# Performance work log

Hardware: AMD Instinct MI355X
Metric: run time of the kernel (lower is better)

Reference implementation:

```python
import jax, jax.numpy as jnp
import numpy as np

N, C, EB, ES = 200000, 2000, 2000000, 40000
LATENT, HIDDEN, EMB = 128, 512, 16
EPS = 1e-4

def _ln(x, g, b):
    m = jnp.mean(x, -1, keepdims=True)
    v = jnp.var(x, -1, keepdims=True)
    return (x - m) / jnp.sqrt(v + 1e-5) * g + b

def _l2norm(x):
    return x / jnp.maximum(jnp.linalg.norm(x, axis=-1, keepdims=True), 1e-12)

def setup_inputs():
    key = jax.random.key(0)
    ks = jax.random.split(key, 10)
    def w(k, shape):
        return jax.random.normal(k, shape, jnp.float32) / np.sqrt(shape[0]).astype(np.float32)
    return dict(
        nodes=jax.random.normal(ks[0], (N, LATENT), jnp.float32),
        clusters=jax.random.randint(ks[1], (N,), 0, C),
        bip_src=jax.random.randint(ks[2], (EB,), 0, N),
        bip_dst=jax.random.randint(ks[3], (EB,), 0, C),
        sup_src=jax.random.randint(ks[4], (ES,), 0, C),
        sup_dst=jax.random.randint(ks[5], (ES,), 0, C),
        cW1=w(ks[6], (LATENT, HIDDEN)), cb1=jnp.zeros((HIDDEN,), jnp.float32),
        cg1=jnp.ones((HIDDEN,), jnp.float32), cbe1=jnp.zeros((HIDDEN,), jnp.float32),
        cW2=w(ks[7], (HIDDEN, EMB)), cb2=jnp.zeros((EMB,), jnp.float32),
        eW1=w(ks[8], (2 * LATENT, HIDDEN)), eb1=jnp.zeros((HIDDEN,), jnp.float32),
        eg1=jnp.ones((HIDDEN,), jnp.float32), ebe1=jnp.zeros((HIDDEN,), jnp.float32),
        eW2=w(ks[9], (HIDDEN, LATENT)), eb2=jnp.zeros((LATENT,), jnp.float32),
        eg2=jnp.ones((LATENT,), jnp.float32), ebe2=jnp.zeros((LATENT,), jnp.float32),
    )

def _forward(nodes, cW1, cb1, cg1, cbe1, cW2, cb2,
             eW1, eb1, eg1, ebe1, eW2, eb2, eg2, ebe2,
             clusters, bip_src, bip_dst, sup_src, sup_dst):
    # clustering network (Linear-LN-ReLU-Linear) + L2 normalize -> [N, EMB]
    emb = jax.nn.relu(_ln(nodes @ cW1 + cb1, cg1, cbe1)) @ cW2 + cb2
    emb = _l2norm(emb)
    # scatter-mean of embeddings per cluster -> supernode centers [C, EMB]
    valid = clusters >= 0
    wgt = valid.astype(emb.dtype)
    cl = jnp.where(valid, clusters, 0)
    sums = jax.ops.segment_sum(emb * wgt[:, None], cl, num_segments=C)
    cnt = jax.ops.segment_sum(wgt, cl, num_segments=C)
    means = _l2norm(sums / jnp.maximum(cnt, 1.0)[:, None])
    # bipartite attention: dot products per edge, min/max-normalized softmax
    # grouped by source node (segment id = bip_src, dim_size = N)
    att = jnp.sum(emb[bip_src] * means[bip_dst], axis=-1)
    amax = jax.ops.segment_max(att, bip_src, num_segments=N)[bip_src]
    amin = jax.ops.segment_min(att, bip_src, num_segments=N)[bip_src]
    att = jnp.exp(2.0 * (att - amin) / (EPS + jax.lax.stop_gradient(amax - amin)))
    bip_att = (att / (EPS + jax.ops.segment_sum(att, bip_src, num_segments=N)[bip_src]))[:, None]
    # supergraph attention: tanh of min/max-normalized dot products,
    # grouped by destination supernode (segment id = sup_dst, dim_size = C)
    satt = jnp.sum(means[sup_src] * means[sup_dst], axis=-1)
    smax = jax.ops.segment_max(satt, sup_dst, num_segments=C)[sup_dst]
    smin = jax.ops.segment_min(satt, sup_dst, num_segments=C)[sup_dst]
    satt = jnp.tanh(2.0 * (satt - smin) / (EPS + jax.lax.stop_gradient(smax - smin)))[:, None]
    # scatter-add raw node features into supernodes, weighted by attention
    supernodes = jax.ops.segment_sum(nodes[bip_src] * bip_att, bip_dst, num_segments=C)
    # superedge encoder (Linear-LN-ReLU-Linear-LN-ReLU) on endpoint concat
    se_in = jnp.concatenate([supernodes[sup_src], supernodes[sup_dst]], axis=1)
    h = jax.nn.relu(_ln(se_in @ eW1 + eb1, eg1, ebe1))
    superedges = jax.nn.relu(_ln(h @ eW2 + eb2, eg2, ebe2))
    return supernodes, superedges, bip_att, satt

def reference(nodes, clusters, bip_src, bip_dst, sup_src, sup_dst,
              cW1, cb1, cg1, cbe1, cW2, cb2,
              eW1, eb1, eg1, ebe1, eW2, eb2, eg2, ebe2):
    return _forward(nodes, cW1, cb1, cg1, cbe1, cW2, cb2,
                    eW1, eb1, eg1, ebe1, eW2, eb2, eg2, ebe2,
                    clusters, bip_src, bip_dst, sup_src, sup_dst)
```

## Files before the change

kernel.cpp:

```cpp
#include <hip/hip_runtime.h>

#define NN 200000
#define CC 2000
#define EBN 2000000
#define ESN 40000
#define EPSA 1e-4f
#define SCH 8000
#define NBKT 1563
#define CVB 1056
#define HSB 977

typedef unsigned short ushort_t;
typedef float f32x4 __attribute__((ext_vector_type(4)));
typedef __bf16 bf16x8 __attribute__((ext_vector_type(8)));
typedef _Float16 f16x8 __attribute__((ext_vector_type(8)));

__device__ __forceinline__ unsigned fenc(float f) {
    unsigned b = __float_as_uint(f);
    return (b & 0x80000000u) ? ~b : (b | 0x80000000u);
}
__device__ __forceinline__ float fdec(unsigned u) {
    return (u & 0x80000000u) ? __uint_as_float(u ^ 0x80000000u) : __uint_as_float(~u);
}
__device__ __forceinline__ unsigned f2bf(float f) {
    unsigned u = __float_as_uint(f);
    return (u + 0x7fffu + ((u >> 16) & 1u)) >> 16;
}
__device__ __forceinline__ float bf2f(ushort_t u) { return __uint_as_float(((unsigned)u) << 16); }
__device__ __forceinline__ ushort_t f2h(float f) {
    const _Float16 h = (_Float16)f;
    return __builtin_bit_cast(ushort_t, h);
}
__device__ __forceinline__ float dot16(const ushort_t* __restrict__ emb_h, const float* __restrict__ means,
                                       int s, int d) {
    const uint4 e0v = *(const uint4*)(emb_h + (size_t)s * 16);
    const uint4 e1v = *(const uint4*)(emb_h + (size_t)s * 16 + 8);
    const float4* mv = (const float4*)(means + (size_t)d * 16);
    const float4 m0 = mv[0], m1 = mv[1], m2 = mv[2], m3 = mv[3];
    float dot = 0.f;
    dot += bf2f((ushort_t)(e0v.x & 0xFFFF)) * m0.x + bf2f((ushort_t)(e0v.x >> 16)) * m0.y;
    dot += bf2f((ushort_t)(e0v.y & 0xFFFF)) * m0.z + bf2f((ushort_t)(e0v.y >> 16)) * m0.w;
    dot += bf2f((ushort_t)(e0v.z & 0xFFFF)) * m1.x + bf2f((ushort_t)(e0v.z >> 16)) * m1.y;
    dot += bf2f((ushort_t)(e0v.w & 0xFFFF)) * m1.z + bf2f((ushort_t)(e0v.w >> 16)) * m1.w;
    dot += bf2f((ushort_t)(e1v.x & 0xFFFF)) * m2.x + bf2f((ushort_t)(e1v.x >> 16)) * m2.y;
    dot += bf2f((ushort_t)(e1v.y & 0xFFFF)) * m2.z + bf2f((ushort_t)(e1v.y >> 16)) * m2.w;
    dot += bf2f((ushort_t)(e1v.z & 0xFFFF)) * m3.x + bf2f((ushort_t)(e1v.z >> 16)) * m3.y;
    dot += bf2f((ushort_t)(e1v.w & 0xFFFF)) * m3.z + bf2f((ushort_t)(e1v.w >> 16)) * m3.w;
    return dot;
}

__global__ __launch_bounds__(256) void k_setup(const float* __restrict__ cW1, const float* __restrict__ cW2,
                                               const float* __restrict__ eW1, const float* __restrict__ eW2,
                                               ushort_t* __restrict__ cW1h, ushort_t* __restrict__ cW2h,
                                               ushort_t* __restrict__ eW1t, ushort_t* __restrict__ eW2t,
                                               const int* __restrict__ bsrc, const int* __restrict__ bdst,
                                               int* __restrict__ hist_d, int* __restrict__ hist_s) {
    __shared__ int hd[CC];
    __shared__ int hs[NBKT];
    if (blockIdx.x < CVB) {
        int id = blockIdx.x * 256 + threadIdx.x;
        if (id < 65536) {
            const int n = id >> 7, k = id & 127;
            cW1h[id] = f2h(cW1[k * 512 + n]);
            return;
        }
        id -= 65536;
        if (id < 8192) {
            const int n = id >> 9, k = id & 511;
            cW2h[id] = f2h(cW2[k * 16 + n]);
            return;
        }
        id -= 8192;
        if (id < 131072) { const int n = id >> 8, k = id & 255; eW1t[id] = (ushort_t)f2bf(eW1[k * 512 + n]); return; }
        id -= 131072;
        if (id < 65536) { const int n = id >> 9, k = id & 511; eW2t[id] = (ushort_t)f2bf(eW2[k * 128 + n]); return; }
        return;
    }
    const int t = threadIdx.x;
    for (int i = t; i < CC; i += 256) hd[i] = 0;
    for (int i = t; i < NBKT; i += 256) hs[i] = 0;
    __syncthreads();
    for (int e = (blockIdx.x - CVB) * 256 + t; e < EBN; e += HSB * 256) {
        atomicAdd(&hd[bdst[e]], 1);
        atomicAdd(&hs[bsrc[e] >> 7], 1);
    }
    __syncthreads();
    for (int i = t; i < CC; i += 256) if (hd[i]) atomicAdd(&hist_d[i], hd[i]);
    for (int i = t; i < NBKT; i += 256) if (hs[i]) atomicAdd(&hist_s[i], hs[i]);
}

__global__ __launch_bounds__(1024) void k_scan2(const int* __restrict__ hist_d, int* __restrict__ offs_d,
                                                int* __restrict__ cursor_d, const int* __restrict__ hist_s,
                                                int* __restrict__ offs_s, int* __restrict__ cursor_s) {
    const int* hist = blockIdx.x ? hist_s : hist_d;
    int* offs = blockIdx.x ? offs_s : offs_d;
    int* cursor = blockIdx.x ? cursor_s : cursor_d;
    const int n = blockIdx.x ? NBKT : CC;
    __shared__ int buf[2][2048];
    const int t = threadIdx.x;
    buf[0][t]        = (t        < n) ? hist[t]        : 0;
    buf[0][t + 1024] = (t + 1024 < n) ? hist[t + 1024] : 0;
    __syncthreads();
    int pp = 0;
    for (int off = 1; off < 2048; off <<= 1) {
        const int np = pp ^ 1;
        for (int i = t; i < 2048; i += 1024) {
            int v = buf[pp][i];
            if (i >= off) v += buf[pp][i - off];
            buf[np][i] = v;
        }
        pp = np;
        __syncthreads();
    }
    for (int i = t; i < n; i += 1024) {
        const int ex = (i == 0) ? 0 : buf[pp][i - 1];
        offs[i] = ex;
        cursor[i] = ex;
    }
}

__global__ __launch_bounds__(256, 3) void k_mlp1(
    const float* __restrict__ nodes, const int* __restrict__ clusters,
    const ushort_t* __restrict__ W1h, const float* __restrict__ b1,
    const float* __restrict__ g1, const float* __restrict__ be1,
    const ushort_t* __restrict__ W2h, const float* __restrict__ b2,
    ushort_t* __restrict__ emb_h, float* __restrict__ sums, float* __restrict__ cnt,
    ushort_t* __restrict__ nodes_h) {
    __shared__ char Ubuf[16384];
    __shared__ float redS[4][32], redQ[4][32];
    ushort_t* Xh = (ushort_t*)Ubuf;
    const int tid = threadIdx.x;
    const int row0 = blockIdx.x * 32;

#pragma unroll
    for (int i = 0; i < 2; ++i) {
        const int c = tid + 256 * i;
        const int row = c >> 4, c8 = c & 15;
        const float4* gp = (const float4*)(nodes + (size_t)(row0 + row) * 128 + c8 * 8);
        const float4 u = gp[0], v = gp[1];
        uint4 pkh;
        pkh.x = f2h(u.x) | ((unsigned)f2h(u.y) << 16);
        pkh.y = f2h(u.z) | ((unsigned)f2h(u.w) << 16);
        pkh.z = f2h(v.x) | ((unsigned)f2h(v.y) << 16);
        pkh.w = f2h(v.z) | ((unsigned)f2h(v.w) << 16);
        const int byte = row * 256 + ((c8 * 16) ^ ((row & 7) << 4));
        *(uint4*)((char*)Xh + byte) = pkh;
        if (nodes_h) {
            uint4 pkb;
            pkb.x = f2bf(u.x) | (f2bf(u.y) << 16);
            pkb.y = f2bf(u.z) | (f2bf(u.w) << 16);
            pkb.z = f2bf(v.x) | (f2bf(v.y) << 16);
            pkb.w = f2bf(v.z) | (f2bf(v.w) << 16);
            ((uint4*)nodes_h)[(size_t)(row0 + row) * 16 + c8] = pkb;
        }
    }
    __syncthreads();

    const int wv = tid >> 6, l = tid & 63;
    const int q = l >> 4, c16 = l & 15;
    const int wcol0 = wv * 128;

    f32x4 acc[2][8];
#pragma unroll
    for (int mt = 0; mt < 2; ++mt)
#pragma unroll
        for (int nt = 0; nt < 8; ++nt) acc[mt][nt] = (f32x4){0.f, 0.f, 0.f, 0.f};

#pragma unroll
    for (int ks = 0; ks < 4; ++ks) {
        f16x8 ah[2];
#pragma unroll
        for (int mt = 0; mt < 2; ++mt) {
            const int row = 16 * mt + c16;
            const int byte = row * 256 + ((64 * ks + 16 * q) ^ ((row & 7) << 4));
            ah[mt] = __builtin_bit_cast(f16x8, *(const uint4*)((const char*)Xh + byte));
        }
#pragma unroll
        for (int nt = 0; nt < 8; ++nt) {
            const int n = wcol0 + 16 * nt + c16;
            const f16x8 bh = __builtin_bit_cast(f16x8, *(const uint4*)(W1h + n * 128 + 32 * ks + 8 * q));
#pragma unroll
            for (int mt = 0; mt < 2; ++mt)
                acc[mt][nt] = __builtin_amdgcn_mfma_f32_16x16x32_f16(ah[mt], bh, acc[mt][nt], 0, 0, 0);
        }
    }

    float b1v[8], g1v[8], bev[8];
#pragma unroll
    for (int nt = 0; nt < 8; ++nt) {
        const int col = wcol0 + 16 * nt + c16;
        b1v[nt] = b1[col]; g1v[nt] = g1[col]; bev[nt] = be1[col];
    }
    float sS[2][4], sQ[2][4];
#pragma unroll
    for (int mt = 0; mt < 2; ++mt)
#pragma unroll
        for (int r = 0; r < 4; ++r) {
            float s = 0.f, qq = 0.f;
#pragma unroll
            for (int nt = 0; nt < 8; ++nt) {
                const float h = acc[mt][nt][r] + b1v[nt];
                acc[mt][nt][r] = h;
                s += h; qq += h * h;
            }
#pragma unroll
            for (int off = 1; off < 16; off <<= 1) {
                s += __shfl_xor(s, off);
                qq += __shfl_xor(qq, off);
            }
            sS[mt][r] = s; sQ[mt][r] = qq;
        }
    if (c16 == 0) {
#pragma unroll
        for (int mt = 0; mt < 2; ++mt)
#pragma unroll
            for (int r = 0; r < 4; ++r) {
                const int row = 16 * mt + 4 * q + r;
                redS[wv][row] = sS[mt][r];
                redQ[wv][row] = sQ[mt][r];
            }
    }
    __syncthreads();

    float mean[2][4], inv[2][4];
#pragma unroll
    for (int mt = 0; mt < 2; ++mt)
#pragma unroll
        for (int r = 0; r < 4; ++r) {
            const int row = 16 * mt + 4 * q + r;
            const float S = redS[0][row] + redS[1][row] + redS[2][row] + redS[3][row];
            const float Q = redQ[0][row] + redQ[1][row] + redQ[2][row] + redQ[3][row];
            const float m_ = S * (1.f / 512.f);
            mean[mt][r] = m_;
            inv[mt][r] = rsqrtf(Q * (1.f / 512.f) - m_ * m_ + 1e-5f);
        }

    ushort_t* Hw = (ushort_t*)(Ubuf + 8192 + wv * 2048);
    f32x4 acc2[2];
    acc2[0] = (f32x4){0.f, 0.f, 0.f, 0.f};
    acc2[1] = (f32x4){0.f, 0.f, 0.f, 0.f};
#pragma unroll
    for (int ch = 0; ch < 4; ++ch) {
#pragma unroll
        for (int mt = 0; mt < 2; ++mt)
#pragma unroll
            for (int r = 0; r < 4; ++r) {
                const int row = 16 * mt + 4 * q + r;
                const int swz = (((row >> 2) & 1) << 3) | (((row >> 3) & 1) << 4);
#pragma unroll
                for (int ntl = 0; ntl < 2; ++ntl) {
                    const int nt = 2 * ch + ntl;
                    const float rv = fmaxf((acc[mt][nt][r] - mean[mt][r]) * inv[mt][r] * g1v[nt] + bev[nt], 0.f);
                    Hw[row * 32 + ((16 * ntl + c16) ^ swz)] = f2h(rv);
                }
            }
        const int kg = wcol0 + 32 * ch + 8 * q;
        const f16x8 bh = __builtin_bit_cast(f16x8, *(const uint4*)(W2h + c16 * 512 + kg));
#pragma unroll
        for (int mt = 0; mt < 2; ++mt) {
            const int row = 16 * mt + c16;
            const int swz = (((row >> 2) & 1) << 3) | (((row >> 3) & 1) << 4);
            const int ci = (8 * q) ^ swz;
            const f16x8 ah = __builtin_bit_cast(f16x8, *(const uint4*)(Hw + row * 32 + ci));
            acc2[mt] = __builtin_amdgcn_mfma_f32_16x16x32_f16(ah, bh, acc2[mt], 0, 0, 0);
        }
    }
    __syncthreads();

    float* Cb = (float*)Ubuf;
#pragma unroll
    for (int mt = 0; mt < 2; ++mt)
#pragma unroll
        for (int r = 0; r < 4; ++r) Cb[(wv * 32 + 16 * mt + 4 * q + r) * 16 + c16] = acc2[mt][r];
    __syncthreads();

#pragma unroll
    for (int rep = 0; rep < 2; ++rep) {
        const int slot = tid + 256 * rep;
        const int row = slot >> 4, col = slot & 15;
        float val = Cb[(0 * 32 + row) * 16 + col] + Cb[(1 * 32 + row) * 16 + col] +
                    Cb[(2 * 32 + row) * 16 + col] + Cb[(3 * 32 + row) * 16 + col] + b2[col];
        float ss = val * val;
#pragma unroll
        for (int off = 1; off < 16; off <<= 1) ss += __shfl_xor(ss, off);
        const float ev = val / fmaxf(sqrtf(ss), 1e-12f);
        const int grow = row0 + row;
        emb_h[(size_t)grow * 16 + col] = (ushort_t)f2bf(ev);
        const int cl = clusters[grow];
        if (cl >= 0) {
            atomicAdd(&sums[cl * 16 + col], ev);
            if (col == 0) atomicAdd(&cnt[cl], 1.f);
        }
    }
}

__global__ __launch_bounds__(256) void k_means(const float* __restrict__ sums, const float* __restrict__ cnt,
                                               float* __restrict__ means) {
    const int t = blockIdx.x * 256 + threadIdx.x;
    const int c = t >> 4;
    const float v = sums[t] / fmaxf(cnt[c], 1.f);
    float sq = v * v;
#pragma unroll
    for (int off = 1; off < 16; off <<= 1) sq += __shfl_xor(sq, off, 16);
    means[t] = v / fmaxf(sqrtf(sq), 1e-12f);
}

__global__ __launch_bounds__(512) void k_bip_sort(const int* __restrict__ src, int* __restrict__ cursor_s,
                                                  unsigned* __restrict__ eid_s) {
    __shared__ int h[NBKT];
    __shared__ int base[NBKT];
    const int t = threadIdx.x;
    const int e0 = blockIdx.x * SCH;
    for (int i = t; i < NBKT; i += 512) h[i] = 0;
    __syncthreads();
    for (int i = t; i < SCH; i += 512) atomicAdd(&h[src[e0 + i] >> 7], 1);
    __syncthreads();
    for (int i = t; i < NBKT; i += 512) {
        const int c = h[i];
        if (c) base[i] = atomicAdd(&cursor_s[i], c);
        h[i] = 0;
    }
    __syncthreads();
    for (int i = t; i < SCH; i += 512) {
        const int e = e0 + i;
        const int s = src[e];
        const int b = s >> 7;
        const int rank = atomicAdd(&h[b], 1);
        eid_s[base[b] + rank] = ((unsigned)(s & 127) << 21) | (unsigned)e;
    }
}

__global__ __launch_bounds__(512) void k_bip_seg(const unsigned* __restrict__ eid_s, const int* __restrict__ offs_s,
                                                 const int* __restrict__ hist_s,
                                                 const int* __restrict__ bdst, const ushort_t* __restrict__ emb_h,
                                                 const float* __restrict__ means, float* __restrict__ att) {
    const int b = blockIdx.x, t = threadIdx.x;
    const int base = offs_s[b], n = hist_s[b];
    const int s0 = b << 7;
    __shared__ unsigned mxs[128], mns[128];
    __shared__ float sms[128];
    if (t < 128) { mxs[t] = 0u; mns[t] = 0xFFFFFFFFu; sms[t] = 0.f; }
    __syncthreads();
    float dv[8];
    int sl[8], ev[8];
#pragma unroll
    for (int k = 0; k < 8; ++k) {
        const int i = k * 512 + t;
        if (i < n) {
            const unsigned pk = eid_s[base + i];
            const int e = (int)(pk & 0x1FFFFFu);
            const int slv = (int)(pk >> 21);
            const int d = bdst[e];
            const float dot = dot16(emb_h, means, s0 + slv, d);
            dv[k] = dot; sl[k] = slv; ev[k] = e;
            const unsigned enc = fenc(dot);
            atomicMax(&mxs[slv], enc);
            atomicMin(&mns[slv], enc);
        }
    }
    for (int i = 4096 + t; i < n; i += 512) {
        const unsigned pk = eid_s[base + i];
        const int e = (int)(pk & 0x1FFFFFu);
        const int slv = (int)(pk >> 21);
        const float dot = dot16(emb_h, means, s0 + slv, bdst[e]);
        const unsigned enc = fenc(dot);
        atomicMax(&mxs[slv], enc);
        atomicMin(&mns[slv], enc);
    }
    __syncthreads();
#pragma unroll
    for (int k = 0; k < 8; ++k) {
        const int i = k * 512 + t;
        if (i < n) {
            const float mx = fdec(mxs[sl[k]]), mn = fdec(mns[sl[k]]);
            const float a = __expf(2.f * (dv[k] - mn) / (EPSA + (mx - mn)));
            dv[k] = a;
            atomicAdd(&sms[sl[k]], a);
        }
    }
    for (int i = 4096 + t; i < n; i += 512) {
        const unsigned pk = eid_s[base + i];
        const int e = (int)(pk & 0x1FFFFFu);
        const int slv = (int)(pk >> 21);
        const float dot = dot16(emb_h, means, s0 + slv, bdst[e]);
        const float mx = fdec(mxs[slv]), mn = fdec(mns[slv]);
        atomicAdd(&sms[slv], __expf(2.f * (dot - mn) / (EPSA + (mx - mn))));
    }
    __syncthreads();
#pragma unroll
    for (int k = 0; k < 8; ++k) {
        const int i = k * 512 + t;
        if (i < n) att[ev[k]] = dv[k] / (EPSA + sms[sl[k]]);
    }
    for (int i = 4096 + t; i < n; i += 512) {
        const unsigned pk = eid_s[base + i];
        const int e = (int)(pk & 0x1FFFFFu);
        const int slv = (int)(pk >> 21);
        const float dot = dot16(emb_h, means, s0 + slv, bdst[e]);
        const float mx = fdec(mxs[slv]), mn = fdec(mns[slv]);
        const float a = __expf(2.f * (dot - mn) / (EPSA + (mx - mn)));
        att[e] = a / (EPSA + sms[slv]);
    }
}

__global__ __launch_bounds__(512) void k_bip_scatter(const int* __restrict__ src, const int* __restrict__ dst,
                                                     const float* __restrict__ att,
                                                     int* __restrict__ cursor, int* __restrict__ src_sorted,
                                                     ushort_t* __restrict__ w_sorted) {
    __shared__ int h[CC];
    __shared__ int base[CC];
    const int t = threadIdx.x;
    const int e0 = blockIdx.x * SCH;
    for (int i = t; i < CC; i += 512) h[i] = 0;
    __syncthreads();
    for (int i = t; i < SCH; i += 512) atomicAdd(&h[dst[e0 + i]], 1);
    __syncthreads();
    for (int i = t; i < CC; i += 512) {
        const int c = h[i];
        if (c) base[i] = atomicAdd(&cursor[i], c);
        h[i] = 0;
    }
    __syncthreads();
    for (int i = t; i < SCH; i += 512) {
        const int e = e0 + i;
        const int s = src[e], d = dst[e];
        const float w = att[e];
        const int rank = atomicAdd(&h[d], 1);
        const int pos = base[d] + rank;
        src_sorted[pos] = s;
        w_sorted[pos] = (ushort_t)f2bf(w);
    }
}

__global__ __launch_bounds__(256) void k_supernode_h(const int* __restrict__ src_sorted,
                                                     const ushort_t* __restrict__ w_sorted,
                                                     const int* __restrict__ offs, const int* __restrict__ hist,
                                                     const ushort_t* __restrict__ nodes_h,
                                                     float* __restrict__ out_sn) {
    const int c = blockIdx.x, t = threadIdx.x;
    const int base = offs[c], n = hist[c];
    const int slot = t >> 5, lane = t & 31;
    const ushort4* nh4 = (const ushort4*)nodes_h;
    float4 aA = make_float4(0.f, 0.f, 0.f, 0.f);
    float4 aB = make_float4(0.f, 0.f, 0.f, 0.f);
    float4 aC = make_float4(0.f, 0.f, 0.f, 0.f);
    float4 aD = make_float4(0.f, 0.f, 0.f, 0.f);
    int i0 = 0;
    for (; i0 + 32 <= n; i0 += 32) {
        {
            const int idx = base + i0 + slot;
            const float w = bf2f(w_sorted[idx]);
            const ushort4 v = nh4[(size_t)src_sorted[idx] * 32 + lane];
            aA.x = fmaf(w, bf2f(v.x), aA.x); aA.y = fmaf(w, bf2f(v.y), aA.y);
            aA.z = fmaf(w, bf2f(v.z), aA.z); aA.w = fmaf(w, bf2f(v.w), aA.w);
        }
        {
            const int idx = base + i0 + 8 + slot;
            const float w = bf2f(w_sorted[idx]);
            const ushort4 v = nh4[(size_t)src_sorted[idx] * 32 + lane];
            aB.x = fmaf(w, bf2f(v.x), aB.x); aB.y = fmaf(w, bf2f(v.y), aB.y);
            aB.z = fmaf(w, bf2f(v.z), aB.z); aB.w = fmaf(w, bf2f(v.w), aB.w);
        }
        {
            const int idx = base + i0 + 16 + slot;
            const float w = bf2f(w_sorted[idx]);
            const ushort4 v = nh4[(size_t)src_sorted[idx] * 32 + lane];
            aC.x = fmaf(w, bf2f(v.x), aC.x); aC.y = fmaf(w, bf2f(v.y), aC.y);
            aC.z = fmaf(w, bf2f(v.z), aC.z); aC.w = fmaf(w, bf2f(v.w), aC.w);
        }
        {
            const int idx = base + i0 + 24 + slot;
            const float w = bf2f(w_sorted[idx]);
            const ushort4 v = nh4[(size_t)src_sorted[idx] * 32 + lane];
            aD.x = fmaf(w, bf2f(v.x), aD.x); aD.y = fmaf(w, bf2f(v.y), aD.y);
            aD.z = fmaf(w, bf2f(v.z), aD.z); aD.w = fmaf(w, bf2f(v.w), aD.w);
        }
    }
    for (; i0 < n; i0 += 8) {
        if (i0 + slot < n) {
            const int idx = base + i0 + slot;
            const float w = bf2f(w_sorted[idx]);
            const ushort4 v = nh4[(size_t)src_sorted[idx] * 32 + lane];
            aA.x = fmaf(w, bf2f(v.x), aA.x); aA.y = fmaf(w, bf2f(v.y), aA.y);
            aA.z = fmaf(w, bf2f(v.z), aA.z); aA.w = fmaf(w, bf2f(v.w), aA.w);
        }
    }
    __shared__ float4 red[256];
    red[t] = make_float4((aA.x + aB.x) + (aC.x + aD.x), (aA.y + aB.y) + (aC.y + aD.y),
                         (aA.z + aB.z) + (aC.z + aD.z), (aA.w + aB.w) + (aC.w + aD.w));
    __syncthreads();
    if (t < 32) {
        float4 r = red[t];
#pragma unroll
        for (int k2 = 1; k2 < 8; ++k2) {
            const float4 o = red[t + 32 * k2];
            r.x += o.x; r.y += o.y; r.z += o.z; r.w += o.w;
        }
        ((float4*)(out_sn + (size_t)c * 128))[t] = r;
    }
}

__global__ __launch_bounds__(256) void k_supernode(const int* __restrict__ src_sorted,
                                                   const ushort_t* __restrict__ w_sorted,
                                                   const int* __restrict__ offs, const int* __restrict__ hist,
                                                   const float* __restrict__ nodes, float* __restrict__ out_sn) {
    const int c = blockIdx.x, t = threadIdx.x;
    const int base = offs[c], n = hist[c];
    const int slot = t >> 5, lane = t & 31;
    const float4* nodes4 = (const float4*)nodes;
    float4 aA = make_float4(0.f, 0.f, 0.f, 0.f);
    int i0 = 0;
    for (; i0 < n; i0 += 8) {
        if (i0 + slot < n) {
            const int idx = base + i0 + slot;
            const float w = bf2f(w_sorted[idx]);
            const float4 v = nodes4[(size_t)src_sorted[idx] * 32 + lane];
            aA.x = fmaf(w, v.x, aA.x); aA.y = fmaf(w, v.y, aA.y);
            aA.z = fmaf(w, v.z, aA.z); aA.w = fmaf(w, v.w, aA.w);
        }
    }
    __shared__ float4 red[256];
    red[t] = aA;
    __syncthreads();
    if (t < 32) {
        float4 r = red[t];
#pragma unroll
        for (int k2 = 1; k2 < 8; ++k2) {
            const float4 o = red[t + 32 * k2];
            r.x += o.x; r.y += o.y; r.z += o.z; r.w += o.w;
        }
        ((float4*)(out_sn + (size_t)c * 128))[t] = r;
    }
}

__global__ __launch_bounds__(256) void k_sup_dot(const int* __restrict__ ss, const int* __restrict__ sd,
                                                 const float* __restrict__ means, float* __restrict__ satt,
                                                 unsigned* __restrict__ smax, unsigned* __restrict__ smin) {
    const int e = blockIdx.x * 256 + threadIdx.x;
    if (e >= ESN) return;
    const int s = ss[e], d = sd[e];
    const float4* av = (const float4*)(means + (size_t)s * 16);
    const float4* bv = (const float4*)(means + (size_t)d * 16);
    float dot = 0.f;
#pragma unroll
    for (int q = 0; q < 4; ++q) {
        const float4 a = av[q], b = bv[q];
        dot += a.x * b.x + a.y * b.y + a.z * b.z + a.w * b.w;
    }
    satt[e] = dot;
    const unsigned enc = fenc(dot);
    atomicMax(&smax[d], enc);
    atomicMin(&smin[d], enc);
}

__global__ __launch_bounds__(256) void k_sup_tanh(const int* __restrict__ sd, float* __restrict__ satt,
                                                  const unsigned* __restrict__ smax,
                                                  const unsigned* __restrict__ smin) {
    const int e = blockIdx.x * 256 + threadIdx.x;
    if (e >= ESN) return;
    const int d = sd[e];
    const float mx = fdec(smax[d]), mn = fdec(smin[d]);
    satt[e] = tanhf(2.f * (satt[e] - mn) / (EPSA + (mx - mn)));
}

__global__ __launch_bounds__(256) void k_edge_mlp(
    const int* __restrict__ esv, const int* __restrict__ edv, const float* __restrict__ sn,
    const ushort_t* __restrict__ W1t, const float* __restrict__ b1, const float* __restrict__ g1,
    const float* __restrict__ be1, const ushort_t* __restrict__ W2t, const float* __restrict__ b2,
    const float* __restrict__ g2, const float* __restrict__ be2, float* __restrict__ out_se) {
    __shared__ ushort_t Xe[32 * 256];
    __shared__ ushort_t Hb[32 * 512];
    __shared__ float redS[4][32], redQ[4][32];
    const int tid = threadIdx.x;
    const int e0 = blockIdx.x * 32;

#pragma unroll
    for (int i = 0; i < 4; ++i) {
        const int c = tid + 256 * i;
        const int row = c >> 5, c8 = c & 31;
        const int node = (c8 < 16) ? esv[e0 + row] : edv[e0 + row];
        const float4* gp = (const float4*)(sn + (size_t)node * 128 + (c8 & 15) * 8);
        const float4 u = gp[0], v = gp[1];
        uint4 pk;
        pk.x = f2bf(u.x) | (f2bf(u.y) << 16);
        pk.y = f2bf(u.z) | (f2bf(u.w) << 16);
        pk.z = f2bf(v.x) | (f2bf(v.y) << 16);
        pk.w = f2bf(v.z) | (f2bf(v.w) << 16);
        const int byte = row * 512 + ((c8 * 16) ^ ((row & 7) << 4));
        *(uint4*)((char*)Xe + byte) = pk;
    }
    __syncthreads();

    const int wv = tid >> 6, l = tid & 63;
    const int q = l >> 4, c16 = l & 15;
    const int wcol0 = wv * 128;

    f32x4 acc[2][8];
#pragma unroll
    for (int mt = 0; mt < 2; ++mt)
#pragma unroll
        for (int nt = 0; nt < 8; ++nt) acc[mt][nt] = (f32x4){0.f, 0.f, 0.f, 0.f};

#pragma unroll
    for (int ks = 0; ks < 8; ++ks) {
        bf16x8 af[2];
#pragma unroll
        for (int mt = 0; mt < 2; ++mt) {
            const int row = 16 * mt + c16;
            const int byte = row * 512 + ((64 * ks + 16 * q) ^ ((row & 7) << 4));
            af[mt] = __builtin_bit_cast(bf16x8, *(const uint4*)((const char*)Xe + byte));
        }
#pragma unroll
        for (int nt = 0; nt < 8; ++nt) {
            const int n = wcol0 + 16 * nt + c16;
            const bf16x8 bfr = __builtin_bit_cast(bf16x8, *(const uint4*)(W1t + n * 256 + 32 * ks + 8 * q));
#pragma unroll
            for (int mt = 0; mt < 2; ++mt)
                acc[mt][nt] = __builtin_amdgcn_mfma_f32_16x16x32_bf16(af[mt], bfr, acc[mt][nt], 0, 0, 0);
        }
    }

    float b1v[8], g1v[8], bev[8];
#pragma unroll
    for (int nt = 0; nt < 8; ++nt) {
        const int col = wcol0 + 16 * nt + c16;
        b1v[nt] = b1[col]; g1v[nt] = g1[col]; bev[nt] = be1[col];
    }
    float sS[2][4], sQ[2][4];
#pragma unroll
    for (int mt = 0; mt < 2; ++mt)
#pragma unroll
        for (int r = 0; r < 4; ++r) {
            float s = 0.f, qq = 0.f;
#pragma unroll
            for (int nt = 0; nt < 8; ++nt) {
                const float h = acc[mt][nt][r] + b1v[nt];
                acc[mt][nt][r] = h;
                s += h; qq += h * h;
            }
#pragma unroll
            for (int off = 1; off < 16; off <<= 1) {
                s += __shfl_xor(s, off);
                qq += __shfl_xor(qq, off);
            }
            sS[mt][r] = s; sQ[mt][r] = qq;
        }
    if (c16 == 0) {
#pragma unroll
        for (int mt = 0; mt < 2; ++mt)
#pragma unroll
            for (int r = 0; r < 4; ++r) {
                const int row = 16 * mt + 4 * q + r;
                redS[wv][row] = sS[mt][r];
                redQ[wv][row] = sQ[mt][r];
            }
    }
    __syncthreads();
#pragma unroll
    for (int mt = 0; mt < 2; ++mt)
#pragma unroll
        for (int r = 0; r < 4; ++r) {
            const int row = 16 * mt + 4 * q + r;
            const float S = redS[0][row] + redS[1][row] + redS[2][row] + redS[3][row];
            const float Q = redQ[0][row] + redQ[1][row] + redQ[2][row] + redQ[3][row];
            const float m_ = S * (1.f / 512.f);
            const float iv = rsqrtf(Q * (1.f / 512.f) - m_ * m_ + 1e-5f);
#pragma unroll
            for (int nt = 0; nt < 8; ++nt) {
                const int col = wcol0 + 16 * nt + c16;
                const float rv = fmaxf((acc[mt][nt][r] - m_) * iv * g1v[nt] + bev[nt], 0.f);
                const int byte = row * 1024 + ((col * 2) ^ ((row & 7) << 4));
                *(ushort_t*)((char*)Hb + byte) = (ushort_t)f2bf(rv);
            }
        }
    __syncthreads();

    f32x4 acc2[2][2];
#pragma unroll
    for (int mt = 0; mt < 2; ++mt)
#pragma unroll
        for (int nt = 0; nt < 2; ++nt) acc2[mt][nt] = (f32x4){0.f, 0.f, 0.f, 0.f};
#pragma unroll 4
    for (int ks = 0; ks < 16; ++ks) {
        bf16x8 bfb[2];
#pragma unroll
        for (int nt = 0; nt < 2; ++nt) {
            const int n = wv * 32 + 16 * nt + c16;
            bfb[nt] = __builtin_bit_cast(bf16x8, *(const uint4*)(W2t + n * 512 + 32 * ks + 8 * q));
        }
#pragma unroll
        for (int mt = 0; mt < 2; ++mt) {
            const int row = 16 * mt + c16;
            const int byte = row * 1024 + ((64 * ks + 16 * q) ^ ((row & 7) << 4));
            const bf16x8 ha = __builtin_bit_cast(bf16x8, *(const uint4*)((const char*)Hb + byte));
#pragma unroll
            for (int nt = 0; nt < 2; ++nt)
                acc2[mt][nt] = __builtin_amdgcn_mfma_f32_16x16x32_bf16(ha, bfb[nt], acc2[mt][nt], 0, 0, 0);
        }
    }

    float b2v[2], g2v[2], be2v[2];
#pragma unroll
    for (int nt = 0; nt < 2; ++nt) {
        const int col = wv * 32 + 16 * nt + c16;
        b2v[nt] = b2[col]; g2v[nt] = g2[col]; be2v[nt] = be2[col];
    }
    float sS2[2][4], sQ2[2][4];
#pragma unroll
    for (int mt = 0; mt < 2; ++mt)
#pragma unroll
        for (int r = 0; r < 4; ++r) {
            float s = 0.f, qq = 0.f;
#pragma unroll
            for (int nt = 0; nt < 2; ++nt) {
                const float h = acc2[mt][nt][r] + b2v[nt];
                acc2[mt][nt][r] = h;
                s += h; qq += h * h;
            }
#pragma unroll
            for (int off = 1; off < 16; off <<= 1) {
                s += __shfl_xor(s, off);
                qq += __shfl_xor(qq, off);
            }
            sS2[mt][r] = s; sQ2[mt][r] = qq;
        }
    __syncthreads();
    if (c16 == 0) {
#pragma unroll
        for (int mt = 0; mt < 2; ++mt)
#pragma unroll
            for (int r = 0; r < 4; ++r) {
                const int row = 16 * mt + 4 * q + r;
                redS[wv][row] = sS2[mt][r];
                redQ[wv][row] = sQ2[mt][r];
            }
    }
    __syncthreads();
#pragma unroll
    for (int mt = 0; mt < 2; ++mt)
#pragma unroll
        for (int r = 0; r < 4; ++r) {
            const int row = 16 * mt + 4 * q + r;
            const float S = redS[0][row] + redS[1][row] + redS[2][row] + redS[3][row];
            const float Q = redQ[0][row] + redQ[1][row] + redQ[2][row] + redQ[3][row];
            const float m_ = S * (1.f / 128.f);
            const float iv = rsqrtf(Q * (1.f / 128.f) - m_ * m_ + 1e-5f);
#pragma unroll
            for (int nt = 0; nt < 2; ++nt) {
                const int col = wv * 32 + 16 * nt + c16;
                const float o = fmaxf((acc2[mt][nt][r] - m_) * iv * g2v[nt] + be2v[nt], 0.f);
                out_se[(size_t)(e0 + row) * 128 + col] = o;
            }
        }
}

extern "C" void kernel_launch(void* const* d_in, const int* in_sizes, int n_in,
                              void* d_out, int out_size, void* d_ws, size_t ws_size,
                              hipStream_t stream) {
    const float* nodes = (const float*)d_in[0];
    const int* clusters = (const int*)d_in[1];
    const int* bsrc = (const int*)d_in[2];
    const int* bdst = (const int*)d_in[3];
    const int* susrc = (const int*)d_in[4];
    const int* sudst = (const int*)d_in[5];
    const float* cW1 = (const float*)d_in[6];
    const float* cb1 = (const float*)d_in[7];
    const float* cg1 = (const float*)d_in[8];
    const float* cbe1 = (const float*)d_in[9];
    const float* cW2 = (const float*)d_in[10];
    const float* cb2 = (const float*)d_in[11];
    const float* eW1 = (const float*)d_in[12];
    const float* eb1 = (const float*)d_in[13];
    const float* eg1 = (const float*)d_in[14];
    const float* ebe1 = (const float*)d_in[15];
    const float* eW2 = (const float*)d_in[16];
    const float* eb2 = (const float*)d_in[17];
    const float* eg2 = (const float*)d_in[18];
    const float* ebe2 = (const float*)d_in[19];

    float* out_sn = (float*)d_out;
    float* out_se = out_sn + (size_t)CC * 128;
    float* out_bip = out_se + (size_t)ESN * 128;
    float* out_satt = out_bip + EBN;

    float* sums = (float*)d_ws;
    float* cnt = sums + 32000;
    int* hist_d = (int*)(cnt + 2000);
    int* hist_s = hist_d + 2000;
    unsigned* smax = (unsigned*)(hist_s + 2000);
    unsigned* smin = smax + 2000;
    ushort_t* emb_h = (ushort_t*)(smin + 2000);
    float* means = (float*)(emb_h + 3200000);
    int* offs_d = (int*)(means + 32000);
    int* cursor_d = offs_d + 2000;
    int* offs_s = cursor_d + 2000;
    int* cursor_s = offs_s + 2000;
    int* src_sorted = cursor_s + 2000;
    ushort_t* w_sorted = (ushort_t*)(src_sorted + 2000000);
    ushort_t* cW1h = w_sorted + 2000000;
    ushort_t* cW1pad = cW1h + 512 * 128;
    ushort_t* cW2h = cW1pad + 512 * 128;
    ushort_t* cW2pad = cW2h + 16 * 512;
    ushort_t* eW1t = cW2pad + 16 * 512;
    ushort_t* eW2t = eW1t + 512 * 256;
    ushort_t* nodes_h = eW2t + 512 * 128;
    unsigned* eid_s = (unsigned*)src_sorted;

    const size_t need_bytes = ((size_t)(char*)(nodes_h + (size_t)NN * 128) - (size_t)(char*)d_ws);
    const bool use_nh = ws_size >= need_bytes;

    hipMemsetAsync(sums, 0, (size_t)(32000 + 2000 + 2000 + 2000 + 2000) * 4, stream);
    hipMemsetAsync(smin, 0xFF, (size_t)2000 * 4, stream);

    k_setup<<<CVB + HSB, 256, 0, stream>>>(cW1, cW2, eW1, eW2, cW1h, cW2h, eW1t, eW2t,
                                           bsrc, bdst, hist_d, hist_s);
    k_scan2<<<2, 1024, 0, stream>>>(hist_d, offs_d, cursor_d, hist_s, offs_s, cursor_s);
    k_mlp1<<<NN / 32, 256, 0, stream>>>(nodes, clusters, cW1h, cb1, cg1, cbe1, cW2h, cb2,
                                        emb_h, sums, cnt, use_nh ? nodes_h : (ushort_t*)nullptr);
    k_means<<<(CC * 16) / 256, 256, 0, stream>>>(sums, cnt, means);
    k_bip_sort<<<EBN / SCH, 512, 0, stream>>>(bsrc, cursor_s, eid_s);
    k_bip_seg<<<NBKT, 512, 0, stream>>>(eid_s, offs_s, hist_s, bdst, emb_h, means, out_bip);
    k_bip_scatter<<<EBN / SCH, 512, 0, stream>>>(bsrc, bdst, out_bip, cursor_d, src_sorted, w_sorted);
    if (use_nh)
        k_supernode_h<<<CC, 256, 0, stream>>>(src_sorted, w_sorted, offs_d, hist_d, nodes_h, out_sn);
    else
        k_supernode<<<CC, 256, 0, stream>>>(src_sorted, w_sorted, offs_d, hist_d, nodes, out_sn);
    k_sup_dot<<<(ESN + 255) / 256, 256, 0, stream>>>(susrc, sudst, means, out_satt, smax, smin);
    k_sup_tanh<<<(ESN + 255) / 256, 256, 0, stream>>>(sudst, out_satt, smax, smin);
    k_edge_mlp<<<ESN / 32, 256, 0, stream>>>(susrc, sudst, out_sn, eW1t, eb1, eg1, ebe1, eW2t, eb2, eg2, ebe2, out_se);
}
```

Baseline: 501.6 us.

## Replace atomic cluster scatter-mean with counting-sort segmented reduction

Removes the global float atomicAdd scatter of embeddings into cluster sums from the MLP kernel. Nodes are instead histogrammed and counting-sorted by cluster in the setup, scan and a new sort kernel, and the MLP writes fp32 embeddings to a buffer. A per-cluster kernel then gathers and reduces them into normalized means. This avoids atomic contention on 2000 clusters and makes the sum deterministic, but adds a sort kernel, an extra 12.8MB fp32 write and a gather pass.

```diff
diff --git a/kernel.cpp b/kernel.cpp
--- a/kernel.cpp
+++ b/kernel.cpp
@@ -54,9 +54,12 @@
                                                ushort_t* __restrict__ cW1h, ushort_t* __restrict__ cW2h,
                                                ushort_t* __restrict__ eW1t, ushort_t* __restrict__ eW2t,
                                                const int* __restrict__ bsrc, const int* __restrict__ bdst,
-                                               int* __restrict__ hist_d, int* __restrict__ hist_s) {
+                                               const int* __restrict__ clusters,
+                                               int* __restrict__ hist_d, int* __restrict__ hist_s,
+                                               int* __restrict__ hist_c) {
     __shared__ int hd[CC];
     __shared__ int hs[NBKT];
+    __shared__ int hc[CC];
     if (blockIdx.x < CVB) {
         int id = blockIdx.x * 256 + threadIdx.x;
         if (id < 65536) {
@@ -77,25 +80,34 @@
         return;
     }
     const int t = threadIdx.x;
-    for (int i = t; i < CC; i += 256) hd[i] = 0;
+    for (int i = t; i < CC; i += 256) { hd[i] = 0; hc[i] = 0; }
     for (int i = t; i < NBKT; i += 256) hs[i] = 0;
     __syncthreads();
     for (int e = (blockIdx.x - CVB) * 256 + t; e < EBN; e += HSB * 256) {
         atomicAdd(&hd[bdst[e]], 1);
         atomicAdd(&hs[bsrc[e] >> 7], 1);
     }
-    __syncthreads();
-    for (int i = t; i < CC; i += 256) if (hd[i]) atomicAdd(&hist_d[i], hd[i]);
+    for (int nidx = (blockIdx.x - CVB) * 256 + t; nidx < NN; nidx += HSB * 256) {
+        const int cl = clusters[nidx];
+        if ((unsigned)cl < CC) atomicAdd(&hc[cl], 1);
+    }
+    __syncthreads();
+    for (int i = t; i < CC; i += 256) {
+        if (hd[i]) atomicAdd(&hist_d[i], hd[i]);
+        if (hc[i]) atomicAdd(&hist_c[i], hc[i]);
+    }
     for (int i = t; i < NBKT; i += 256) if (hs[i]) atomicAdd(&hist_s[i], hs[i]);
 }
 
-__global__ __launch_bounds__(1024) void k_scan2(const int* __restrict__ hist_d, int* __restrict__ offs_d,
+__global__ __launch_bounds__(1024) void k_scan3(const int* __restrict__ hist_d, int* __restrict__ offs_d,
                                                 int* __restrict__ cursor_d, const int* __restrict__ hist_s,
-                                                int* __restrict__ offs_s, int* __restrict__ cursor_s) {
-    const int* hist = blockIdx.x ? hist_s : hist_d;
-    int* offs = blockIdx.x ? offs_s : offs_d;
-    int* cursor = blockIdx.x ? cursor_s : cursor_d;
-    const int n = blockIdx.x ? NBKT : CC;
+                                                int* __restrict__ offs_s, int* __restrict__ cursor_s,
+                                                const int* __restrict__ hist_c, int* __restrict__ offs_c,
+                                                int* __restrict__ cursor_c) {
+    const int* hist = (blockIdx.x == 0) ? hist_d : (blockIdx.x == 1) ? hist_s : hist_c;
+    int* offs = (blockIdx.x == 0) ? offs_d : (blockIdx.x == 1) ? offs_s : offs_c;
+    int* cursor = (blockIdx.x == 0) ? cursor_d : (blockIdx.x == 1) ? cursor_s : cursor_c;
+    const int n = (blockIdx.x == 1) ? NBKT : CC;
     __shared__ int buf[2][2048];
     const int t = threadIdx.x;
     buf[0][t]        = (t        < n) ? hist[t]        : 0;
@@ -119,13 +131,40 @@
     }
 }
 
+__global__ __launch_bounds__(512) void k_nsort(const int* __restrict__ clusters, int* __restrict__ cursor_c,
+                                               int* __restrict__ nid_sorted) {
+    __shared__ int h[CC];
+    __shared__ int base[CC];
+    const int t = threadIdx.x;
+    const int n0 = blockIdx.x * 8000;
+    for (int i = t; i < CC; i += 512) h[i] = 0;
+    __syncthreads();
+    for (int i = t; i < 8000; i += 512) {
+        const int cl = clusters[n0 + i];
+        if ((unsigned)cl < CC) atomicAdd(&h[cl], 1);
+    }
+    __syncthreads();
+    for (int i = t; i < CC; i += 512) {
+        const int c = h[i];
+        if (c) base[i] = atomicAdd(&cursor_c[i], c);
+        h[i] = 0;
+    }
+    __syncthreads();
+    for (int i = t; i < 8000; i += 512) {
+        const int cl = clusters[n0 + i];
+        if ((unsigned)cl < CC) {
+            const int r = atomicAdd(&h[cl], 1);
+            nid_sorted[base[cl] + r] = n0 + i;
+        }
+    }
+}
+
 __global__ __launch_bounds__(256, 3) void k_mlp1(
-    const float* __restrict__ nodes, const int* __restrict__ clusters,
+    const float* __restrict__ nodes,
     const ushort_t* __restrict__ W1h, const float* __restrict__ b1,
     const float* __restrict__ g1, const float* __restrict__ be1,
     const ushort_t* __restrict__ W2h, const float* __restrict__ b2,
-    ushort_t* __restrict__ emb_h, float* __restrict__ sums, float* __restrict__ cnt,
-    ushort_t* __restrict__ nodes_h) {
+    ushort_t* __restrict__ emb_h, float* __restrict__ emb_f, ushort_t* __restrict__ nodes_h) {
     __shared__ char Ubuf[16384];
     __shared__ float redS[4][32], redQ[4][32];
     ushort_t* Xh = (ushort_t*)Ubuf;
@@ -284,25 +323,36 @@
 #pragma unroll
         for (int off = 1; off < 16; off <<= 1) ss += __shfl_xor(ss, off);
         const float ev = val / fmaxf(sqrtf(ss), 1e-12f);
-        const int grow = row0 + row;
-        emb_h[(size_t)grow * 16 + col] = (ushort_t)f2bf(ev);
-        const int cl = clusters[grow];
-        if (cl >= 0) {
-            atomicAdd(&sums[cl * 16 + col], ev);
-            if (col == 0) atomicAdd(&cnt[cl], 1.f);
-        }
-    }
-}
-
-__global__ __launch_bounds__(256) void k_means(const float* __restrict__ sums, const float* __restrict__ cnt,
-                                               float* __restrict__ means) {
-    const int t = blockIdx.x * 256 + threadIdx.x;
-    const int c = t >> 4;
-    const float v = sums[t] / fmaxf(cnt[c], 1.f);
-    float sq = v * v;
-#pragma unroll
-    for (int off = 1; off < 16; off <<= 1) sq += __shfl_xor(sq, off, 16);
-    means[t] = v / fmaxf(sqrtf(sq), 1e-12f);
+        const size_t gidx = (size_t)(row0 + row) * 16 + col;
+        emb_h[gidx] = (ushort_t)f2bf(ev);
+        emb_f[gidx] = ev;
+    }
+}
+
+__global__ __launch_bounds__(128) void k_cmeans(const int* __restrict__ nid_sorted, const int* __restrict__ offs_c,
+                                                const int* __restrict__ hist_c, const float* __restrict__ emb_f,
+                                                float* __restrict__ means) {
+    const int c = blockIdx.x, t = threadIdx.x;
+    const int base = offs_c[c], n = hist_c[c];
+    const int slot = t >> 4, lane = t & 15;
+    float s = 0.f;
+    for (int i = slot; i < n; i += 8) {
+        const int nid = nid_sorted[base + i];
+        s += emb_f[(size_t)nid * 16 + lane];
+    }
+    __shared__ float red[8][16];
+    red[slot][lane] = s;
+    __syncthreads();
+    if (t < 16) {
+        float v = 0.f;
+#pragma unroll
+        for (int k = 0; k < 8; ++k) v += red[k][t];
+        v /= fmaxf((float)n, 1.f);
+        float sq = v * v;
+#pragma unroll
+        for (int off = 1; off < 16; off <<= 1) sq += __shfl_xor(sq, off, 16);
+        means[c * 16 + t] = v / fmaxf(sqrtf(sq), 1e-12f);
+    }
 }
 
 __global__ __launch_bounds__(512) void k_bip_sort(const int* __restrict__ src, int* __restrict__ cursor_s,
@@ -783,19 +833,22 @@
     float* out_bip = out_se + (size_t)ESN * 128;
     float* out_satt = out_bip + EBN;
 
-    float* sums = (float*)d_ws;
-    float* cnt = sums + 32000;
-    int* hist_d = (int*)(cnt + 2000);
+    int* hist_d = (int*)d_ws;
     int* hist_s = hist_d + 2000;
-    unsigned* smax = (unsigned*)(hist_s + 2000);
+    int* hist_c = hist_s + 2000;
+    unsigned* smax = (unsigned*)(hist_c + 2000);
     unsigned* smin = smax + 2000;
     ushort_t* emb_h = (ushort_t*)(smin + 2000);
-    float* means = (float*)(emb_h + 3200000);
+    float* emb_f = (float*)(emb_h + 3200000);
+    float* means = emb_f + 3200000;
     int* offs_d = (int*)(means + 32000);
     int* cursor_d = offs_d + 2000;
     int* offs_s = cursor_d + 2000;
     int* cursor_s = offs_s + 2000;
-    int* src_sorted = cursor_s + 2000;
+    int* offs_c = cursor_s + 2000;
+    int* cursor_c = offs_c + 2000;
+    int* nid_sorted = cursor_c + 2000;
+    int* src_sorted = nid_sorted + 200000;
     ushort_t* w_sorted = (ushort_t*)(src_sorted + 2000000);
     ushort_t* cW1h = w_sorted + 2000000;
     ushort_t* cW1pad = cW1h + 512 * 128;
@@ -809,15 +862,17 @@
     const size_t need_bytes = ((size_t)(char*)(nodes_h + (size_t)NN * 128) - (size_t)(char*)d_ws);
     const bool use_nh = ws_size >= need_bytes;
 
-    hipMemsetAsync(sums, 0, (size_t)(32000 + 2000 + 2000 + 2000 + 2000) * 4, stream);
+    hipMemsetAsync(hist_d, 0, (size_t)(2000 + 2000 + 2000 + 2000) * 4, stream);
     hipMemsetAsync(smin, 0xFF, (size_t)2000 * 4, stream);
 
     k_setup<<<CVB + HSB, 256, 0, stream>>>(cW1, cW2, eW1, eW2, cW1h, cW2h, eW1t, eW2t,
-                                           bsrc, bdst, hist_d, hist_s);
-    k_scan2<<<2, 1024, 0, stream>>>(hist_d, offs_d, cursor_d, hist_s, offs_s, cursor_s);
-    k_mlp1<<<NN / 32, 256, 0, stream>>>(nodes, clusters, cW1h, cb1, cg1, cbe1, cW2h, cb2,
-                                        emb_h, sums, cnt, use_nh ? nodes_h : (ushort_t*)nullptr);
-    k_means<<<(CC * 16) / 256, 256, 0, stream>>>(sums, cnt, means);
+                                           bsrc, bdst, clusters, hist_d, hist_s, hist_c);
+    k_scan3<<<3, 1024, 0, stream>>>(hist_d, offs_d, cursor_d, hist_s, offs_s, cursor_s,
+                                    hist_c, offs_c, cursor_c);
+    k_nsort<<<NN / 8000, 512, 0, stream>>>(clusters, cursor_c, nid_sorted);
+    k_mlp1<<<NN / 32, 256, 0, stream>>>(nodes, cW1h, cb1, cg1, cbe1, cW2h, cb2,
+                                        emb_h, emb_f, use_nh ? nodes_h : (ushort_t*)nullptr);
+    k_cmeans<<<CC, 128, 0, stream>>>(nid_sorted, offs_c, hist_c, emb_f, means);
     k_bip_sort<<<EBN / SCH, 512, 0, stream>>>(bsrc, cursor_s, eid_s);
     k_bip_seg<<<NBKT, 512, 0, stream>>>(eid_s, offs_s, hist_s, bdst, emb_h, means, out_bip);
     k_bip_scatter<<<EBN / SCH, 512, 0, stream>>>(bsrc, bdst, out_bip, cursor_d, src_sorted, w_sorted);
```

Measured after the change: 521.7 us. 1.04x slower.
